# Performance work log

Hardware: AMD Instinct MI355X
Metric: run time of the kernel (lower is better)

Reference implementation:

```python
import jax, jax.numpy as jnp
import numpy as np

IN_DIM, HID, MID, FFN, OUT = 384, 128, 1024, 512, 1024
B, T = 8, 4096
LN_EPS = 1e-5


def _legs_hippo(n: int) -> np.ndarray:
    # A[i, j] = P_i(2j/n - 1) * sqrt(2i + 1), Legendre via 3-term recurrence
    x = 2.0 * np.arange(n) / n - 1.0          # eval points, shape [n]
    P = np.zeros((n, n), dtype=np.float64)     # P[i] = P_i(x)
    P[0] = 1.0
    if n > 1:
        P[1] = x
    for i in range(1, n - 1):
        P[i + 1] = ((2 * i + 1) * x * P[i] - i * P[i - 1]) / (i + 1)
    A = P * np.sqrt(2.0 * np.arange(n) + 1.0)[:, None]
    # rescale so the 4096-step recurrence stays finite (A is a free Parameter,
    # so any test value is valid; unscaled LegS overflows fp32 in ~20 steps)
    s = np.linalg.norm(A, 2)
    return (A / (1.05 * s)).astype(np.float32)


def _layernorm(x, g, b):
    mu = jnp.mean(x, axis=-1, keepdims=True)
    var = jnp.var(x, axis=-1, keepdims=True)
    return (x - mu) * jax.lax.rsqrt(var + LN_EPS) * g + b


def setup_inputs() -> dict:
    key = jax.random.key(0)
    ks = jax.random.split(key, 16)

    def w(k, shape, fan_in):
        return jax.random.normal(k, shape, jnp.float32) * (1.0 / np.sqrt(fan_in))

    return {
        "padded_x": jax.random.normal(ks[0], (B, T, IN_DIM), jnp.float32),
        "seq_lens": jax.random.randint(ks[1], (B,), 1, T + 1, jnp.int32),
        "A": jnp.asarray(_legs_hippo(HID)),
        "enc_w1": w(ks[2], (IN_DIM, MID), IN_DIM), "enc_b1": jnp.zeros((MID,), jnp.float32),
        "enc_w2": w(ks[3], (MID, HID), MID), "enc_b2": jnp.zeros((HID,), jnp.float32),
        "proj_w": w(ks[4], (HID, MID), HID), "proj_b": jnp.zeros((MID,), jnp.float32),
        "ln1_g": jnp.ones((MID,), jnp.float32), "ln1_b": jnp.zeros((MID,), jnp.float32),
        "ffn_w1": w(ks[5], (MID, FFN), MID), "ffn_b1": jnp.zeros((FFN,), jnp.float32),
        "ffn_w2": w(ks[6], (FFN, OUT), FFN), "ffn_b2": jnp.zeros((OUT,), jnp.float32),
        "ln2_g": jnp.ones((OUT,), jnp.float32), "ln2_b": jnp.zeros((OUT,), jnp.float32),
        "out_w": w(ks[7], (OUT, OUT), OUT), "out_b": jnp.zeros((OUT,), jnp.float32),
    }


def reference(padded_x, seq_lens, A, enc_w1, enc_b1, enc_w2, enc_b2,
              proj_w, proj_b, ln1_g, ln1_b, ffn_w1, ffn_b1, ffn_w2, ffn_b2,
              ln2_g, ln2_b, out_w, out_b):
    # encoder: Linear -> GELU(exact) -> Linear   [B, T, HID]
    h_mid = jax.nn.gelu(padded_x @ enc_w1 + enc_b1, approximate=False)
    seqs_bx = h_mid @ enc_w2 + enc_b2

    # masked linear recurrence h_t = A @ h_{t-1} + Bx_t via lax.scan over time
    xs = jnp.swapaxes(seqs_bx, 0, 1)           # [T, B, HID]
    ts = jnp.arange(xs.shape[0])

    def step(h, inp):
        x_t, t = inp
        upd = h @ A.T + x_t                     # (A @ h)^T batched
        mask = (t < seq_lens)[:, None]          # [B, 1]
        return jnp.where(mask, upd, h), None

    h0 = jnp.zeros((padded_x.shape[0], A.shape[0]), padded_x.dtype)
    batch_h, _ = jax.lax.scan(step, h0, (xs, ts))

    # decoder
    projected = batch_h @ proj_w + proj_b
    norm_h = _layernorm(projected, ln1_g, ln1_b)
    ffn_out = jax.nn.gelu(norm_h @ ffn_w1 + ffn_b1, approximate=False) @ ffn_w2 + ffn_b2
    ffn_out = ffn_out + projected               # residual (requires OUT == MID)
    norm_ffn = _layernorm(ffn_out, ln2_g, ln2_b)
    return norm_ffn @ out_w + out_b             # [B, OUT]
```

## Files before the change

kernel.cpp:

```cpp
#include <hip/hip_runtime.h>

typedef __attribute__((ext_vector_type(8))) short short8;
typedef __attribute__((ext_vector_type(4))) short short4v;
typedef __attribute__((ext_vector_type(4))) float float4v;

__device__ __forceinline__ float bf2f(short s) {
  union { float f; unsigned u; } cv; cv.u = ((unsigned)(unsigned short)s) << 16; return cv.f;
}
__device__ __forceinline__ short f2bf(float f) {
  union { float f; unsigned u; } cv; cv.f = f;
  unsigned u = cv.u;
  unsigned r = u + 0x7FFFu + ((u >> 16) & 1u);
  return (short)(r >> 16);
}
__device__ __forceinline__ float gelu_f(float v) {
  return 0.5f * v * (1.0f + erff(v * 0.70710678118654752440f));
}
__device__ __forceinline__ void glds16(const short* g, short* l) {
  __builtin_amdgcn_global_load_lds(
      (const __attribute__((address_space(1))) void*)g,
      (__attribute__((address_space(3))) void*)l, 16, 0, 0);
}

__global__ __launch_bounds__(256) void enc_fused(
    const short* __restrict__ xB, const short* __restrict__ w1T,
    const short* __restrict__ w2T, const float* __restrict__ b1,
    float* __restrict__ encP, const int* __restrict__ seq_lens)
{
  int m0 = blockIdx.x * 64;
  { int b = m0 >> 12, t = m0 & 4095; if (t >= seq_lens[b]) return; }
  int nc0 = blockIdx.y * 2;

  __shared__ __align__(16) short As[64 * 64];
  __shared__ __align__(16) short Ws[128 * 64];
  __shared__ __align__(16) short midb[64 * 128];

  int tid = threadIdx.x, lane = tid & 63, wave = tid >> 6;
  int l15 = lane & 15, quad = lane >> 4;
  int lr = lane >> 3, lseg = lane & 7;

  float4v accO[4][2];
#pragma unroll
  for (int i = 0; i < 4; i++)
#pragma unroll
    for (int j = 0; j < 2; j++) accO[i][j] = 0;

  for (int nci = 0; nci < 2; ++nci) {
    int nc = nc0 + nci;
    float4v accM[4][2];
#pragma unroll
    for (int i = 0; i < 4; i++)
#pragma unroll
      for (int j = 0; j < 2; j++) accM[i][j] = 0;

    for (int ks = 0; ks < 6; ++ks) {
      int kk = ks * 64;
#pragma unroll
      for (int i = 0; i < 2; i++) {
        int rowg = wave * 16 + i * 8;
        glds16(xB + (size_t)(m0 + rowg + lr) * 384 + kk + (lseg ^ lr) * 8, &As[rowg * 64]);
      }
#pragma unroll
      for (int i = 0; i < 4; i++) {
        int rowg = wave * 32 + i * 8;
        glds16(w1T + (size_t)(nc * 128 + rowg + lr) * 384 + kk + (lseg ^ lr) * 8, &Ws[rowg * 64]);
      }
      __syncthreads();
#pragma unroll
      for (int kh = 0; kh < 2; kh++) {
        int s = kh * 4 + quad;
        short8 af[4], bfr[2];
#pragma unroll
        for (int im = 0; im < 4; im++) {
          int r = im * 16 + l15;
          af[im] = *(short8*)&As[r * 64 + ((s ^ (r & 7)) * 8)];
        }
#pragma unroll
        for (int in = 0; in < 2; in++) {
          int r = wave * 32 + in * 16 + l15;
          bfr[in] = *(short8*)&Ws[r * 64 + ((s ^ (r & 7)) * 8)];
        }
#pragma unroll
        for (int im = 0; im < 4; im++)
#pragma unroll
          for (int in = 0; in < 2; in++)
            accM[im][in] = __builtin_amdgcn_mfma_f32_16x16x32_bf16(af[im], bfr[in], accM[im][in], 0, 0, 0);
      }
      __syncthreads();
    }
#pragma unroll
    for (int im = 0; im < 4; im++)
#pragma unroll
      for (int in = 0; in < 2; in++) {
        int k = wave * 32 + in * 16 + l15;
        float bias = b1[nc * 128 + k];
#pragma unroll
        for (int reg = 0; reg < 4; reg++) {
          int m = im * 16 + quad * 4 + reg;
          float v = gelu_f(accM[im][in][reg] + bias);
          int s = k >> 3;
          int sw = (s & 8) | ((s & 7) ^ (m & 7));
          midb[m * 128 + sw * 8 + (k & 7)] = f2bf(v);
        }
      }
    __syncthreads();
#pragma unroll
    for (int ks2 = 0; ks2 < 2; ++ks2) {
      int kk = nc * 128 + ks2 * 64;
#pragma unroll
      for (int i = 0; i < 4; i++) {
        int rowg = wave * 32 + i * 8;
        glds16(w2T + (size_t)(rowg + lr) * 1024 + kk + (lseg ^ lr) * 8, &Ws[rowg * 64]);
      }
      __syncthreads();
#pragma unroll
      for (int kh = 0; kh < 2; kh++) {
        short8 af[4], bfr[2];
#pragma unroll
        for (int im = 0; im < 4; im++) {
          int m = im * 16 + l15;
          int kb = ks2 * 64 + kh * 32 + quad * 8;
          int s = kb >> 3;
          int sw = (s & 8) | ((s & 7) ^ (m & 7));
          af[im] = *(short8*)&midb[m * 128 + sw * 8];
        }
#pragma unroll
        for (int in = 0; in < 2; in++) {
          int r = wave * 32 + in * 16 + l15;
          int s = kh * 4 + quad;
          bfr[in] = *(short8*)&Ws[r * 64 + ((s ^ (r & 7)) * 8)];
        }
#pragma unroll
        for (int im = 0; im < 4; im++)
#pragma unroll
          for (int in = 0; in < 2; in++)
            accO[im][in] = __builtin_amdgcn_mfma_f32_16x16x32_bf16(af[im], bfr[in], accO[im][in], 0, 0, 0);
      }
      __syncthreads();
    }
  }
  float* outp = encP + ((size_t)blockIdx.y << 22);
#pragma unroll
  for (int im = 0; im < 4; im++)
#pragma unroll
    for (int in = 0; in < 2; in++) {
      int n = wave * 32 + in * 16 + l15;
#pragma unroll
      for (int reg = 0; reg < 4; reg++) {
        int m = m0 + im * 16 + quad * 4 + reg;
        outp[(size_t)m * 128 + n] = accO[im][in][reg];
      }
    }
}

__global__ __launch_bounds__(256) void enc_reduce(
    const float* __restrict__ encP, const float* __restrict__ b2,
    short* __restrict__ seqs, const int* __restrict__ seq_lens)
{
  int m0 = blockIdx.x * 64;
  { int b = m0 >> 12, t = m0 & 4095; if (t >= seq_lens[b]) return; }
  int t = threadIdx.x;
#pragma unroll
  for (int i = 0; i < 8; i++) {
    int f4 = t + i * 256;
    int m = m0 + (f4 >> 5);
    int cg = f4 & 31;
    size_t off = (size_t)m * 128 + cg * 4;
    float4v v = *(const float4v*)&encP[off];
#pragma unroll
    for (int y = 1; y < 4; y++) {
      float4v w = *(const float4v*)&encP[((size_t)y << 22) + off];
#pragma unroll
      for (int q = 0; q < 4; q++) v[q] += w[q];
    }
    float4v bb = *(const float4v*)&b2[cg * 4];
    short4v o;
#pragma unroll
    for (int q = 0; q < 4; q++) o[q] = f2bf(v[q] + bb[q]);
    *(short4v*)&seqs[off] = o;
  }
}

__global__ __launch_bounds__(256) void gemm_bt(
    const short* __restrict__ A_, const short* __restrict__ BT,
    float* __restrict__ out, int lda, int ldb, int ldc,
    int kSteps, int kChunk)
{
  int m0 = blockIdx.y * 128;
  int n0 = blockIdx.x * 128;
  int kBase = blockIdx.z * kChunk;

  __shared__ __align__(16) short As[128 * 64];
  __shared__ __align__(16) short Bs[128 * 64];

  int tid = threadIdx.x;
  int lane = tid & 63, wave = tid >> 6;
  int l15 = lane & 15, quad = lane >> 4;
  int wm = wave & 1, wn = wave >> 1;
  int lr = lane >> 3, lseg = lane & 7;

  float4v acc[4][4];
#pragma unroll
  for (int i = 0; i < 4; i++)
#pragma unroll
    for (int j = 0; j < 4; j++) acc[i][j] = 0;

  for (int ks = 0; ks < kSteps; ++ks) {
    int kk = kBase + ks * 64;
#pragma unroll
    for (int i = 0; i < 4; i++) {
      int rowg = wave * 32 + i * 8;
      glds16(A_ + (size_t)(m0 + rowg + lr) * lda + kk + (lseg ^ lr) * 8, &As[rowg * 64]);
      glds16(BT + (size_t)(n0 + rowg + lr) * ldb + kk + (lseg ^ lr) * 8, &Bs[rowg * 64]);
    }
    __syncthreads();
#pragma unroll
    for (int kh = 0; kh < 2; kh++) {
      int s = kh * 4 + quad;
      short8 af[4], bfr[4];
#pragma unroll
      for (int im = 0; im < 4; im++) {
        int r = wm * 64 + im * 16 + l15;
        af[im] = *(short8*)&As[r * 64 + ((s ^ (r & 7)) * 8)];
      }
#pragma unroll
      for (int in = 0; in < 4; in++) {
        int r = wn * 64 + in * 16 + l15;
        bfr[in] = *(short8*)&Bs[r * 64 + ((s ^ (r & 7)) * 8)];
      }
#pragma unroll
      for (int im = 0; im < 4; im++)
#pragma unroll
        for (int in = 0; in < 4; in++)
          acc[im][in] = __builtin_amdgcn_mfma_f32_16x16x32_bf16(af[im], bfr[in], acc[im][in], 0, 0, 0);
    }
    __syncthreads();
  }
  float* outz = out + (size_t)blockIdx.z * 65536;
#pragma unroll
  for (int im = 0; im < 4; im++)
#pragma unroll
    for (int in = 0; in < 4; in++) {
      int n = n0 + wn * 64 + in * 16 + l15;
#pragma unroll
      for (int reg = 0; reg < 4; reg++) {
        int m = m0 + wm * 64 + im * 16 + quad * 4 + reg;
        outz[(size_t)m * ldc + n] = acc[im][in][reg];
      }
    }
}

__global__ void prep_wide(const float* __restrict__ x, const float* __restrict__ w1,
                          const float* __restrict__ w2,
                          const float* __restrict__ proj_w, const float* __restrict__ ffn_w1,
                          const float* __restrict__ ffn_w2, const float* __restrict__ out_w,
                          const float* __restrict__ A, const int* __restrict__ seq_lens,
                          short* __restrict__ xB,
                          short* __restrict__ w1T, short* __restrict__ w2T,
                          short* __restrict__ projB, short* __restrict__ ffn1B,
                          short* __restrict__ ffn2B, short* __restrict__ outB,
                          short* __restrict__ P1, short* __restrict__ P1t,
                          short* __restrict__ P2t,
                          short* __restrict__ Spow, short* __restrict__ SpowT)
{
  int idx = blockIdx.x * 256 + threadIdx.x;
  if (idx < 3145728) {
    int row = idx / 96;
    int t = row & 4095, b = row >> 12;
    if (t >= seq_lens[b]) return;
    float4v v = ((const float4v*)x)[idx];
    short4v o;
#pragma unroll
    for (int j = 0; j < 4; j++) o[j] = f2bf(v[j]);
    ((short4v*)xB)[idx] = o;
    return;
  }
  idx -= 3145728;
  if (idx < 393216) {
    int n = idx / 384, k = idx % 384;
    w1T[idx] = f2bf(w1[k * 1024 + n]);
    return;
  }
  idx -= 393216;
  if (idx < 131072) {
    int n = idx / 1024, k = idx % 1024;
    w2T[idx] = f2bf(w2[k * 128 + n]);
    return;
  }
  idx -= 131072;
  if (idx < 131072) { projB[idx] = f2bf(proj_w[idx]); return; }
  idx -= 131072;
  if (idx < 524288) { ffn1B[idx] = f2bf(ffn_w1[idx]); return; }
  idx -= 524288;
  if (idx < 524288) { ffn2B[idx] = f2bf(ffn_w2[idx]); return; }
  idx -= 524288;
  if (idx < 1048576) { outB[idx] = f2bf(out_w[idx]); return; }
  idx -= 1048576;
  if (idx < 16384) {
    int i = idx >> 7, j = idx & 127;
    short bidv = f2bf((i == j) ? 1.0f : 0.0f);
    P1[i * 8192 + 63 * 128 + j] = bidv;
    P1t[(63 * 128 + j) * 128 + i] = bidv;
    P2t[(63 * 128 + j) * 128 + i] = bidv;
    short ab = f2bf(A[idx]);
    Spow[idx] = ab;
    SpowT[(size_t)j * 128 + i] = ab;
  }
}

__global__ __launch_bounds__(256) void pow_chain(short* __restrict__ Spow,
                                                 short* __restrict__ SpowT)
{
  __shared__ short X[16384];
  __shared__ short XT[16384];
  int t = threadIdx.x;
  for (int i = t * 8; i < 16384; i += 2048) {
    *(short8*)&X[i]  = *(const short8*)&Spow[i];
    *(short8*)&XT[i] = *(const short8*)&SpowT[i];
  }
  __syncthreads();
  int lane = t & 63, wave = t >> 6, l15 = lane & 15, quad = lane >> 4;
  for (int step = 1; step <= 11; ++step) {
    short8 af[2][4], bfr[8][4];
#pragma unroll
    for (int mt = 0; mt < 2; mt++)
#pragma unroll
      for (int ks = 0; ks < 4; ks++)
        af[mt][ks] = *(short8*)&X[(wave * 32 + mt * 16 + l15) * 128 + ks * 32 + quad * 8];
#pragma unroll
    for (int nt = 0; nt < 8; nt++)
#pragma unroll
      for (int ks = 0; ks < 4; ks++)
        bfr[nt][ks] = *(short8*)&XT[(nt * 16 + l15) * 128 + ks * 32 + quad * 8];
    __syncthreads();
    float4v acc[2][8];
#pragma unroll
    for (int mt = 0; mt < 2; mt++)
#pragma unroll
      for (int nt = 0; nt < 8; nt++) acc[mt][nt] = 0;
#pragma unroll
    for (int ks = 0; ks < 4; ks++)
#pragma unroll
      for (int mt = 0; mt < 2; mt++)
#pragma unroll
        for (int nt = 0; nt < 8; nt++)
          acc[mt][nt] = __builtin_amdgcn_mfma_f32_16x16x32_bf16(af[mt][ks], bfr[nt][ks], acc[mt][nt], 0, 0, 0);
    short* gX  = Spow  + (size_t)step * 16384;
    short* gXT = SpowT + (size_t)step * 16384;
#pragma unroll
    for (int mt = 0; mt < 2; mt++)
#pragma unroll
      for (int nt = 0; nt < 8; nt++)
#pragma unroll
        for (int reg = 0; reg < 4; reg++) {
          int m = wave * 32 + mt * 16 + quad * 4 + reg;
          int n = nt * 16 + l15;
          short v = f2bf(acc[mt][nt][reg]);
          X[m * 128 + n] = v; XT[n * 128 + m] = v;
          gX[m * 128 + n] = v; gXT[n * 128 + m] = v;
        }
    __syncthreads();
  }
}

__global__ __launch_bounds__(256) void pow_fill(const short* __restrict__ Spow,
                                                const short* __restrict__ SpowT,
                                                short* __restrict__ P1,
                                                short* __restrict__ P1t,
                                                short* __restrict__ P2t)
{
  __shared__ short cur[16384];
  __shared__ short Bt[16384];
  int bid = blockIdx.x;
  int table1 = bid < 63;
  int e = table1 ? bid + 1 : bid - 62;
  int t = threadIdx.x;
  int lane = t & 63, wave = t >> 6, l15 = lane & 15, quad = lane >> 4;

  int bits = e;
  int k0 = __ffs(bits) - 1; bits &= bits - 1;
  int s0 = table1 ? k0 : (k0 == 0 ? 6 : 6 + k0);
  for (int i = t * 8; i < 16384; i += 2048)
    *(short8*)&cur[i] = *(const short8*)&Spow[(size_t)s0 * 16384 + i];

  while (bits) {
    int k = __ffs(bits) - 1; bits &= bits - 1;
    int si = table1 ? k : (k == 0 ? 6 : 6 + k);
    for (int i = t * 8; i < 16384; i += 2048)
      *(short8*)&Bt[i] = *(const short8*)&SpowT[(size_t)si * 16384 + i];
    __syncthreads();
    short8 af[2][4], bfr[8][4];
#pragma unroll
    for (int mt = 0; mt < 2; mt++)
#pragma unroll
      for (int ks = 0; ks < 4; ks++)
        af[mt][ks] = *(short8*)&cur[(wave * 32 + mt * 16 + l15) * 128 + ks * 32 + quad * 8];
#pragma unroll
    for (int nt = 0; nt < 8; nt++)
#pragma unroll
      for (int ks = 0; ks < 4; ks++)
        bfr[nt][ks] = *(short8*)&Bt[(nt * 16 + l15) * 128 + ks * 32 + quad * 8];
    __syncthreads();
    float4v acc[2][8];
#pragma unroll
    for (int mt = 0; mt < 2; mt++)
#pragma unroll
      for (int nt = 0; nt < 8; nt++) acc[mt][nt] = 0;
#pragma unroll
    for (int ks = 0; ks < 4; ks++)
#pragma unroll
      for (int mt = 0; mt < 2; mt++)
#pragma unroll
        for (int nt = 0; nt < 8; nt++)
          acc[mt][nt] = __builtin_amdgcn_mfma_f32_16x16x32_bf16(af[mt][ks], bfr[nt][ks], acc[mt][nt], 0, 0, 0);
#pragma unroll
    for (int mt = 0; mt < 2; mt++)
#pragma unroll
      for (int nt = 0; nt < 8; nt++)
#pragma unroll
        for (int reg = 0; reg < 4; reg++) {
          int m = wave * 32 + mt * 16 + quad * 4 + reg;
          int n = nt * 16 + l15;
          cur[m * 128 + n] = f2bf(acc[mt][nt][reg]);
        }
    __syncthreads();
  }
  __syncthreads();
  int slot = 63 - e;
  for (int idx = t; idx < 16384; idx += 256) {
    int i = idx >> 7, j = idx & 127;
    short v = cur[idx];
    if (table1) {
      P1[i * 8192 + slot * 128 + j] = v;
      P1t[(slot * 128 + j) * 128 + i] = v;
    } else {
      P2t[(slot * 128 + j) * 128 + i] = v;
    }
  }
}

__global__ __launch_bounds__(256) void combine_gemm(
    const float* __restrict__ Vz, const short* __restrict__ seqs,
    const int* __restrict__ seq_lens,
    const short* __restrict__ P2t, const short* __restrict__ P1t,
    float* __restrict__ hFtail)
{
  __shared__ short X[256 * 8];
  int pp = blockIdx.x >> 5, ks = blockIdx.x & 31;
  int t = threadIdx.x;
  for (int e = t; e < 2048; e += 256) {
    int klocal = e >> 3, b = e & 7;
    int cp = ks * 2 + (klocal >> 7), i = klocal & 127;
    int L = seq_lens[b];
    if (pp == 0) {
      int F = L >> 6, sh = 64 - F;
      float v = 0.f;
      if (cp >= sh) {
        int row = (b * 64 + (cp - sh)) * 128 + i;
#pragma unroll
        for (int z = 0; z < 32; z++) v += Vz[(size_t)z * 65536 + row];
      }
      X[e] = f2bf(v);
    } else {
      int F = L >> 6, rr = L & 63, sh = 64 - rr;
      short s = 0;
      if (cp >= sh) s = seqs[((size_t)b * 4096 + F * 64 + (cp - sh)) * 128 + i];
      X[e] = s;
    }
  }
  __syncthreads();
  const short* P = pp ? P1t : P2t;
  float* outp = hFtail + pp * 1024;
  int i = t & 127, g = t >> 7;
  float acc[4] = {0, 0, 0, 0};
  for (int kl = 0; kl < 256; ++kl) {
    int k = ks * 256 + kl;
    float pv = bf2f(P[k * 128 + i]);
    short4v xv = *(const short4v*)(X + kl * 8 + g * 4);
#pragma unroll
    for (int q = 0; q < 4; q++) acc[q] += bf2f(xv[q]) * pv;
  }
#pragma unroll
  for (int q = 0; q < 4; q++) atomicAdd(&outp[(g * 4 + q) * 128 + i], acc[q]);
}

__global__ __launch_bounds__(256) void proj_stage(
    const float* __restrict__ hFtail, const short* __restrict__ P1t,
    const int* __restrict__ seq_lens, const short* __restrict__ projB,
    const float* __restrict__ proj_b, float* __restrict__ projected)
{
  __shared__ short hT[128 * 8];
  __shared__ float red[4][64][8];
  int t = threadIdx.x;
  {
    int b = t >> 5, i4 = (t & 31) * 4;
    int rr = seq_lens[b] & 63;
    const short* M = P1t + (size_t)(63 - rr) * 128 * 128;
    const float* hF = hFtail + b * 128;
    float acc[4];
#pragma unroll
    for (int q = 0; q < 4; q++) acc[q] = hFtail[1024 + b * 128 + i4 + q];
    for (int j = 0; j < 128; ++j) {
      float hv = hF[j];
      short4v mv = *(const short4v*)&M[j * 128 + i4];
#pragma unroll
      for (int q = 0; q < 4; q++) acc[q] += bf2f(mv[q]) * hv;
    }
#pragma unroll
    for (int q = 0; q < 4; q++) hT[(i4 + q) * 8 + b] = f2bf(acc[q]);
  }
  __syncthreads();
  int c = t & 63, sl = t >> 6;
  int n = blockIdx.x * 64 + c;
  float acc[8] = {0, 0, 0, 0, 0, 0, 0, 0};
  for (int k = sl * 32; k < sl * 32 + 32; ++k) {
    short8 xv = *(short8*)&hT[k * 8];
    float wv = bf2f(projB[k * 1024 + n]);
#pragma unroll
    for (int b = 0; b < 8; b++) acc[b] += bf2f(xv[b]) * wv;
  }
#pragma unroll
  for (int b = 0; b < 8; b++) red[sl][c][b] = acc[b];
  __syncthreads();
  if (sl == 0) {
#pragma unroll
    for (int s = 1; s < 4; s++)
#pragma unroll
      for (int b = 0; b < 8; b++) acc[b] += red[s][c][b];
    float bn = proj_b[n];
#pragma unroll
    for (int b = 0; b < 8; b++) projected[b * 1024 + n] = acc[b] + bn;
  }
}

__global__ __launch_bounds__(256) void ffn1_stage(
    const float* __restrict__ projected, const float* __restrict__ g1,
    const float* __restrict__ b1, const short* __restrict__ ffn1B,
    float* __restrict__ ffn1raw)
{
  __shared__ float part[8][32][2];
  __shared__ float stats[8][2];
  __shared__ short xT[256 * 8];
  __shared__ float red[4][64][8];
  int t = threadIdx.x;
  { int b = t >> 5, j0 = t & 31; float s = 0, q = 0;
    for (int k = j0 * 32; k < j0 * 32 + 32; ++k) { float v = projected[b * 1024 + k]; s += v; q += v * v; }
    part[b][j0][0] = s; part[b][j0][1] = q; }
  __syncthreads();
  if (t < 8) {
    float s = 0, q = 0;
    for (int j = 0; j < 32; j++) { s += part[t][j][0]; q += part[t][j][1]; }
    float mu = s * (1.0f / 1024.0f);
    float var = q * (1.0f / 1024.0f) - mu * mu;
    stats[t][0] = mu; stats[t][1] = rsqrtf(var + 1e-5f);
  }
  __syncthreads();
  int ky0 = blockIdx.y * 256;
  for (int idx = t; idx < 2048; idx += 256) {
    int kl = idx >> 3, b = idx & 7; int k = ky0 + kl;
    float v = (projected[b * 1024 + k] - stats[b][0]) * stats[b][1] * g1[k] + b1[k];
    xT[kl * 8 + b] = f2bf(v);
  }
  __syncthreads();
  int c = t & 63, sl = t >> 6;
  int n = blockIdx.x * 64 + c;
  float acc[8] = {0, 0, 0, 0, 0, 0, 0, 0};
  for (int kl = sl * 64; kl < sl * 64 + 64; ++kl) {
    short8 xv = *(short8*)&xT[kl * 8];
    float wv = bf2f(ffn1B[(size_t)(ky0 + kl) * 512 + n]);
#pragma unroll
    for (int b = 0; b < 8; b++) acc[b] += bf2f(xv[b]) * wv;
  }
#pragma unroll
  for (int b = 0; b < 8; b++) red[sl][c][b] = acc[b];
  __syncthreads();
  if (sl == 0) {
#pragma unroll
    for (int s = 1; s < 4; s++)
#pragma unroll
      for (int b = 0; b < 8; b++) acc[b] += red[s][c][b];
#pragma unroll
    for (int b = 0; b < 8; b++) atomicAdd(&ffn1raw[b * 512 + n], acc[b]);
  }
}

__global__ __launch_bounds__(256) void ffn2_stage(
    const float* __restrict__ ffn1raw, const float* __restrict__ fb1,
    const short* __restrict__ ffn2B, float* __restrict__ ffn2raw)
{
  __shared__ short xT[256 * 8];
  __shared__ float red[4][64][8];
  int t = threadIdx.x;
  int ky0 = blockIdx.y * 256;
  for (int idx = t; idx < 2048; idx += 256) {
    int kl = idx >> 3, b = idx & 7; int k = ky0 + kl;
    float v = gelu_f(ffn1raw[b * 512 + k] + fb1[k]);
    xT[kl * 8 + b] = f2bf(v);
  }
  __syncthreads();
  int c = t & 63, sl = t >> 6;
  int n = blockIdx.x * 64 + c;
  float acc[8] = {0, 0, 0, 0, 0, 0, 0, 0};
  for (int kl = sl * 64; kl < sl * 64 + 64; ++kl) {
    short8 xv = *(short8*)&xT[kl * 8];
    float wv = bf2f(ffn2B[(size_t)(ky0 + kl) * 1024 + n]);
#pragma unroll
    for (int b = 0; b < 8; b++) acc[b] += bf2f(xv[b]) * wv;
  }
#pragma unroll
  for (int b = 0; b < 8; b++) red[sl][c][b] = acc[b];
  __syncthreads();
  if (sl == 0) {
#pragma unroll
    for (int s = 1; s < 4; s++)
#pragma unroll
      for (int b = 0; b < 8; b++) acc[b] += red[s][c][b];
#pragma unroll
    for (int b = 0; b < 8; b++) atomicAdd(&ffn2raw[b * 1024 + n], acc[b]);
  }
}

__global__ __launch_bounds__(256) void out_stage(
    const float* __restrict__ ffn2raw, const float* __restrict__ fb2,
    const float* __restrict__ projected, const float* __restrict__ g2,
    const float* __restrict__ b2ln, const short* __restrict__ outB,
    const float* __restrict__ out_b, float* __restrict__ d_out)
{
  __shared__ float part[8][32][2];
  __shared__ float stats[8][2];
  __shared__ short xT[512 * 8];
  __shared__ float red[4][64][8];
  int t = threadIdx.x;
  { int b = t >> 5, j0 = t & 31; float s = 0, q = 0;
    for (int k = j0 * 32; k < j0 * 32 + 32; ++k) {
      float v = ffn2raw[b * 1024 + k] + fb2[k] + projected[b * 1024 + k];
      s += v; q += v * v;
    }
    part[b][j0][0] = s; part[b][j0][1] = q; }
  __syncthreads();
  if (t < 8) {
    float s = 0, q = 0;
    for (int j = 0; j < 32; j++) { s += part[t][j][0]; q += part[t][j][1]; }
    float mu = s * (1.0f / 1024.0f);
    float var = q * (1.0f / 1024.0f) - mu * mu;
    stats[t][0] = mu; stats[t][1] = rsqrtf(var + 1e-5f);
  }
  __syncthreads();
  int ky0 = blockIdx.y * 512;
  for (int idx = t; idx < 4096; idx += 256) {
    int kl = idx >> 3, b = idx & 7; int k = ky0 + kl;
    float v = ffn2raw[b * 1024 + k] + fb2[k] + projected[b * 1024 + k];
    v = (v - stats[b][0]) * stats[b][1] * g2[k] + b2ln[k];
    xT[kl * 8 + b] = f2bf(v);
  }
  __syncthreads();
  int c = t & 63, sl = t >> 6;
  int n = blockIdx.x * 64 + c;
  float acc[8] = {0, 0, 0, 0, 0, 0, 0, 0};
  for (int kl = sl * 128; kl < sl * 128 + 128; ++kl) {
    short8 xv = *(short8*)&xT[kl * 8];
    float wv = bf2f(outB[(size_t)(ky0 + kl) * 1024 + n]);
#pragma unroll
    for (int b = 0; b < 8; b++) acc[b] += bf2f(xv[b]) * wv;
  }
#pragma unroll
  for (int b = 0; b < 8; b++) red[sl][c][b] = acc[b];
  __syncthreads();
  if (sl == 0) {
#pragma unroll
    for (int s = 1; s < 4; s++)
#pragma unroll
      for (int b = 0; b < 8; b++) acc[b] += red[s][c][b];
    float bn = (blockIdx.y == 0) ? out_b[n] : 0.0f;
#pragma unroll
    for (int b = 0; b < 8; b++) atomicAdd(&d_out[b * 1024 + n], acc[b] + bn);
  }
}

extern "C" void kernel_launch(void* const* d_in, const int* in_sizes, int n_in,
                              void* d_out, int out_size, void* d_ws, size_t ws_size,
                              hipStream_t stream)
{
  (void)in_sizes; (void)n_in; (void)out_size; (void)ws_size;
  const float* x      = (const float*)d_in[0];
  const int* seq_lens = (const int*)d_in[1];
  const float* A      = (const float*)d_in[2];
  const float* enc_w1 = (const float*)d_in[3];
  const float* enc_b1 = (const float*)d_in[4];
  const float* enc_w2 = (const float*)d_in[5];
  const float* enc_b2 = (const float*)d_in[6];
  const float* proj_w = (const float*)d_in[7];
  const float* proj_b = (const float*)d_in[8];
  const float* ln1_g  = (const float*)d_in[9];
  const float* ln1_b  = (const float*)d_in[10];
  const float* ffn_w1 = (const float*)d_in[11];
  const float* ffn_b1 = (const float*)d_in[12];
  const float* ffn_w2 = (const float*)d_in[13];
  const float* ffn_b2 = (const float*)d_in[14];
  const float* ln2_g  = (const float*)d_in[15];
  const float* ln2_b  = (const float*)d_in[16];
  const float* out_w  = (const float*)d_in[17];
  const float* out_b  = (const float*)d_in[18];

  char* p = (char*)d_ws;
  auto alloc = [&](size_t bytes) { char* r = p; p += (bytes + 255) & ~(size_t)255; return r; };
  short* xB    = (short*)alloc(32768ull * 384 * 2);
  float* encP  = (float*)alloc(4ull * 32768 * 128 * 4);
  short* seqs  = (short*)alloc(32768ull * 128 * 2);
  short* w1T   = (short*)alloc(1024ull * 384 * 2);
  short* w2T   = (short*)alloc(128ull * 1024 * 2);
  short* projB = (short*)alloc(128ull * 1024 * 2);
  short* ffn1B = (short*)alloc(1024ull * 512 * 2);
  short* ffn2B = (short*)alloc(512ull * 1024 * 2);
  short* outB  = (short*)alloc(1024ull * 1024 * 2);
  short* Spow  = (short*)alloc(12ull * 16384 * 2);
  short* SpowT = (short*)alloc(12ull * 16384 * 2);
  short* P1    = (short*)alloc(128ull * 8192 * 2);
  short* P1t   = (short*)alloc(8192ull * 128 * 2);
  short* P2t   = (short*)alloc(8192ull * 128 * 2);
  float* Vz    = (float*)alloc(32ull * 512 * 128 * 4);
  float* hFtail  = (float*)alloc(2ull * 8 * 128 * 4);
  float* ffn1raw = (float*)alloc(8ull * 512 * 4);
  float* ffn2raw = (float*)alloc(8ull * 1024 * 4);
  float* projected = (float*)alloc(8ull * 1024 * 4);

  hipMemsetAsync(hFtail, 0, (2ull * 8 * 128 + 8ull * 512 + 8ull * 1024) * 4, stream);
  hipMemsetAsync(d_out, 0, 8192ull * 4, stream);

  prep_wide<<<23104, 256, 0, stream>>>(x, enc_w1, enc_w2, proj_w, ffn_w1, ffn_w2, out_w, A,
      seq_lens, xB, w1T, w2T, projB, ffn1B, ffn2B, outB, P1, P1t, P2t, Spow, SpowT);
  pow_chain<<<1, 256, 0, stream>>>(Spow, SpowT);
  pow_fill<<<126, 256, 0, stream>>>(Spow, SpowT, P1, P1t, P2t);

  enc_fused<<<dim3(512, 4), 256, 0, stream>>>(xB, w1T, w2T, enc_b1, encP, seq_lens);
  enc_reduce<<<512, 256, 0, stream>>>(encP, enc_b2, seqs, seq_lens);

  gemm_bt<<<dim3(1, 4, 32), 256, 0, stream>>>(seqs, P1, Vz, 8192, 8192, 128, 4, 256);
  combine_gemm<<<64, 256, 0, stream>>>(Vz, seqs, seq_lens, P2t, P1t, hFtail);

  proj_stage<<<16, 256, 0, stream>>>(hFtail, P1t, seq_lens, projB, proj_b, projected);
  ffn1_stage<<<dim3(8, 4), 256, 0, stream>>>(projected, ln1_g, ln1_b, ffn1B, ffn1raw);
  ffn2_stage<<<dim3(16, 2), 256, 0, stream>>>(ffn1raw, ffn_b1, ffn2B, ffn2raw);
  out_stage<<<dim3(16, 2), 256, 0, stream>>>(ffn2raw, ffn_b2, projected, ln2_g, ln2_b,
      outB, out_b, (float*)d_out);
}
```

Before: 405.4 us.

## Fuse encoder reduce into last block, drop memsets, widen decoder grids

Several changes land together. The encoder split-N reduction is folded into enc_fused: the last of the four column blocks per row tile, found with an atomic counter, sums the partials and writes the bf16 sequence, which removes the enc_reduce launch. The two memsets are replaced by zeroing inside prep_wide, and the encoder's shared memory is reduced by aliasing the input tile onto the mid buffer. The decoder GEMV stages and combine_gemm are split across more blocks with smaller K chunks to raise parallelism, and the pow_chain/pow_fill transposed stores are vectorized or coalesced. The cost is extra atomics, threadfences and more atomicAdd traffic into the outputs.

```diff
diff --git a/kernel.cpp b/kernel.cpp
--- a/kernel.cpp
+++ b/kernel.cpp
@@ -20,234 +20,6 @@
   __builtin_amdgcn_global_load_lds(
       (const __attribute__((address_space(1))) void*)g,
       (__attribute__((address_space(3))) void*)l, 16, 0, 0);
-}
-
-__global__ __launch_bounds__(256) void enc_fused(
-    const short* __restrict__ xB, const short* __restrict__ w1T,
-    const short* __restrict__ w2T, const float* __restrict__ b1,
-    float* __restrict__ encP, const int* __restrict__ seq_lens)
-{
-  int m0 = blockIdx.x * 64;
-  { int b = m0 >> 12, t = m0 & 4095; if (t >= seq_lens[b]) return; }
-  int nc0 = blockIdx.y * 2;
-
-  __shared__ __align__(16) short As[64 * 64];
-  __shared__ __align__(16) short Ws[128 * 64];
-  __shared__ __align__(16) short midb[64 * 128];
-
-  int tid = threadIdx.x, lane = tid & 63, wave = tid >> 6;
-  int l15 = lane & 15, quad = lane >> 4;
-  int lr = lane >> 3, lseg = lane & 7;
-
-  float4v accO[4][2];
-#pragma unroll
-  for (int i = 0; i < 4; i++)
-#pragma unroll
-    for (int j = 0; j < 2; j++) accO[i][j] = 0;
-
-  for (int nci = 0; nci < 2; ++nci) {
-    int nc = nc0 + nci;
-    float4v accM[4][2];
-#pragma unroll
-    for (int i = 0; i < 4; i++)
-#pragma unroll
-      for (int j = 0; j < 2; j++) accM[i][j] = 0;
-
-    for (int ks = 0; ks < 6; ++ks) {
-      int kk = ks * 64;
-#pragma unroll
-      for (int i = 0; i < 2; i++) {
-        int rowg = wave * 16 + i * 8;
-        glds16(xB + (size_t)(m0 + rowg + lr) * 384 + kk + (lseg ^ lr) * 8, &As[rowg * 64]);
-      }
-#pragma unroll
-      for (int i = 0; i < 4; i++) {
-        int rowg = wave * 32 + i * 8;
-        glds16(w1T + (size_t)(nc * 128 + rowg + lr) * 384 + kk + (lseg ^ lr) * 8, &Ws[rowg * 64]);
-      }
-      __syncthreads();
-#pragma unroll
-      for (int kh = 0; kh < 2; kh++) {
-        int s = kh * 4 + quad;
-        short8 af[4], bfr[2];
-#pragma unroll
-        for (int im = 0; im < 4; im++) {
-          int r = im * 16 + l15;
-          af[im] = *(short8*)&As[r * 64 + ((s ^ (r & 7)) * 8)];
-        }
-#pragma unroll
-        for (int in = 0; in < 2; in++) {
-          int r = wave * 32 + in * 16 + l15;
-          bfr[in] = *(short8*)&Ws[r * 64 + ((s ^ (r & 7)) * 8)];
-        }
-#pragma unroll
-        for (int im = 0; im < 4; im++)
-#pragma unroll
-          for (int in = 0; in < 2; in++)
-            accM[im][in] = __builtin_amdgcn_mfma_f32_16x16x32_bf16(af[im], bfr[in], accM[im][in], 0, 0, 0);
-      }
-      __syncthreads();
-    }
-#pragma unroll
-    for (int im = 0; im < 4; im++)
-#pragma unroll
-      for (int in = 0; in < 2; in++) {
-        int k = wave * 32 + in * 16 + l15;
-        float bias = b1[nc * 128 + k];
-#pragma unroll
-        for (int reg = 0; reg < 4; reg++) {
-          int m = im * 16 + quad * 4 + reg;
-          float v = gelu_f(accM[im][in][reg] + bias);
-          int s = k >> 3;
-          int sw = (s & 8) | ((s & 7) ^ (m & 7));
-          midb[m * 128 + sw * 8 + (k & 7)] = f2bf(v);
-        }
-      }
-    __syncthreads();
-#pragma unroll
-    for (int ks2 = 0; ks2 < 2; ++ks2) {
-      int kk = nc * 128 + ks2 * 64;
-#pragma unroll
-      for (int i = 0; i < 4; i++) {
-        int rowg = wave * 32 + i * 8;
-        glds16(w2T + (size_t)(rowg + lr) * 1024 + kk + (lseg ^ lr) * 8, &Ws[rowg * 64]);
-      }
-      __syncthreads();
-#pragma unroll
-      for (int kh = 0; kh < 2; kh++) {
-        short8 af[4], bfr[2];
-#pragma unroll
-        for (int im = 0; im < 4; im++) {
-          int m = im * 16 + l15;
-          int kb = ks2 * 64 + kh * 32 + quad * 8;
-          int s = kb >> 3;
-          int sw = (s & 8) | ((s & 7) ^ (m & 7));
-          af[im] = *(short8*)&midb[m * 128 + sw * 8];
-        }
-#pragma unroll
-        for (int in = 0; in < 2; in++) {
-          int r = wave * 32 + in * 16 + l15;
-          int s = kh * 4 + quad;
-          bfr[in] = *(short8*)&Ws[r * 64 + ((s ^ (r & 7)) * 8)];
-        }
-#pragma unroll
-        for (int im = 0; im < 4; im++)
-#pragma unroll
-          for (int in = 0; in < 2; in++)
-            accO[im][in] = __builtin_amdgcn_mfma_f32_16x16x32_bf16(af[im], bfr[in], accO[im][in], 0, 0, 0);
-      }
-      __syncthreads();
-    }
-  }
-  float* outp = encP + ((size_t)blockIdx.y << 22);
-#pragma unroll
-  for (int im = 0; im < 4; im++)
-#pragma unroll
-    for (int in = 0; in < 2; in++) {
-      int n = wave * 32 + in * 16 + l15;
-#pragma unroll
-      for (int reg = 0; reg < 4; reg++) {
-        int m = m0 + im * 16 + quad * 4 + reg;
-        outp[(size_t)m * 128 + n] = accO[im][in][reg];
-      }
-    }
-}
-
-__global__ __launch_bounds__(256) void enc_reduce(
-    const float* __restrict__ encP, const float* __restrict__ b2,
-    short* __restrict__ seqs, const int* __restrict__ seq_lens)
-{
-  int m0 = blockIdx.x * 64;
-  { int b = m0 >> 12, t = m0 & 4095; if (t >= seq_lens[b]) return; }
-  int t = threadIdx.x;
-#pragma unroll
-  for (int i = 0; i < 8; i++) {
-    int f4 = t + i * 256;
-    int m = m0 + (f4 >> 5);
-    int cg = f4 & 31;
-    size_t off = (size_t)m * 128 + cg * 4;
-    float4v v = *(const float4v*)&encP[off];
-#pragma unroll
-    for (int y = 1; y < 4; y++) {
-      float4v w = *(const float4v*)&encP[((size_t)y << 22) + off];
-#pragma unroll
-      for (int q = 0; q < 4; q++) v[q] += w[q];
-    }
-    float4v bb = *(const float4v*)&b2[cg * 4];
-    short4v o;
-#pragma unroll
-    for (int q = 0; q < 4; q++) o[q] = f2bf(v[q] + bb[q]);
-    *(short4v*)&seqs[off] = o;
-  }
-}
-
-__global__ __launch_bounds__(256) void gemm_bt(
-    const short* __restrict__ A_, const short* __restrict__ BT,
-    float* __restrict__ out, int lda, int ldb, int ldc,
-    int kSteps, int kChunk)
-{
-  int m0 = blockIdx.y * 128;
-  int n0 = blockIdx.x * 128;
-  int kBase = blockIdx.z * kChunk;
-
-  __shared__ __align__(16) short As[128 * 64];
-  __shared__ __align__(16) short Bs[128 * 64];
-
-  int tid = threadIdx.x;
-  int lane = tid & 63, wave = tid >> 6;
-  int l15 = lane & 15, quad = lane >> 4;
-  int wm = wave & 1, wn = wave >> 1;
-  int lr = lane >> 3, lseg = lane & 7;
-
-  float4v acc[4][4];
-#pragma unroll
-  for (int i = 0; i < 4; i++)
-#pragma unroll
-    for (int j = 0; j < 4; j++) acc[i][j] = 0;
-
-  for (int ks = 0; ks < kSteps; ++ks) {
-    int kk = kBase + ks * 64;
-#pragma unroll
-    for (int i = 0; i < 4; i++) {
-      int rowg = wave * 32 + i * 8;
-      glds16(A_ + (size_t)(m0 + rowg + lr) * lda + kk + (lseg ^ lr) * 8, &As[rowg * 64]);
-      glds16(BT + (size_t)(n0 + rowg + lr) * ldb + kk + (lseg ^ lr) * 8, &Bs[rowg * 64]);
-    }
-    __syncthreads();
-#pragma unroll
-    for (int kh = 0; kh < 2; kh++) {
-      int s = kh * 4 + quad;
-      short8 af[4], bfr[4];
-#pragma unroll
-      for (int im = 0; im < 4; im++) {
-        int r = wm * 64 + im * 16 + l15;
-        af[im] = *(short8*)&As[r * 64 + ((s ^ (r & 7)) * 8)];
-      }
-#pragma unroll
-      for (int in = 0; in < 4; in++) {
-        int r = wn * 64 + in * 16 + l15;
-        bfr[in] = *(short8*)&Bs[r * 64 + ((s ^ (r & 7)) * 8)];
-      }
-#pragma unroll
-      for (int im = 0; im < 4; im++)
-#pragma unroll
-        for (int in = 0; in < 4; in++)
-          acc[im][in] = __builtin_amdgcn_mfma_f32_16x16x32_bf16(af[im], bfr[in], acc[im][in], 0, 0, 0);
-    }
-    __syncthreads();
-  }
-  float* outz = out + (size_t)blockIdx.z * 65536;
-#pragma unroll
-  for (int im = 0; im < 4; im++)
-#pragma unroll
-    for (int in = 0; in < 4; in++) {
-      int n = n0 + wn * 64 + in * 16 + l15;
-#pragma unroll
-      for (int reg = 0; reg < 4; reg++) {
-        int m = m0 + wm * 64 + im * 16 + quad * 4 + reg;
-        outz[(size_t)m * ldc + n] = acc[im][in][reg];
-      }
-    }
 }
 
 __global__ void prep_wide(const float* __restrict__ x, const float* __restrict__ w1,
@@ -261,7 +33,10 @@
                           short* __restrict__ ffn2B, short* __restrict__ outB,
                           short* __restrict__ P1, short* __restrict__ P1t,
                           short* __restrict__ P2t,
-                          short* __restrict__ Spow, short* __restrict__ SpowT)
+                          short* __restrict__ Spow, short* __restrict__ SpowT,
+                          float* __restrict__ hFtail, float* __restrict__ ffn1raw,
+                          float* __restrict__ ffn2raw, float* __restrict__ dout0,
+                          int* __restrict__ encCnt)
 {
   int idx = blockIdx.x * 256 + threadIdx.x;
   if (idx < 3145728) {
@@ -298,13 +73,183 @@
   idx -= 1048576;
   if (idx < 16384) {
     int i = idx >> 7, j = idx & 127;
-    short bidv = f2bf((i == j) ? 1.0f : 0.0f);
-    P1[i * 8192 + 63 * 128 + j] = bidv;
-    P1t[(63 * 128 + j) * 128 + i] = bidv;
-    P2t[(63 * 128 + j) * 128 + i] = bidv;
+    short idv = f2bf((i == j) ? 1.0f : 0.0f);
+    P1[i * 8192 + 63 * 128 + j] = idv;
+    P1t[(63 * 128 + j) * 128 + i] = idv;
+    P2t[(63 * 128 + j) * 128 + i] = idv;
     short ab = f2bf(A[idx]);
     Spow[idx] = ab;
     SpowT[(size_t)j * 128 + i] = ab;
+    return;
+  }
+  idx -= 16384;
+  if (idx < 2048) { hFtail[idx] = 0.f; return; }
+  idx -= 2048;
+  if (idx < 4096) { ffn1raw[idx] = 0.f; return; }
+  idx -= 4096;
+  if (idx < 8192) { ffn2raw[idx] = 0.f; return; }
+  idx -= 8192;
+  if (idx < 8192) { dout0[idx] = 0.f; return; }
+  idx -= 8192;
+  if (idx < 512) encCnt[idx] = 0;
+}
+
+__global__ __launch_bounds__(256) void enc_fused(
+    const short* __restrict__ xB, const short* __restrict__ w1T,
+    const short* __restrict__ w2T, const float* __restrict__ b1,
+    const float* __restrict__ b2, float* __restrict__ encP,
+    short* __restrict__ seqs, int* __restrict__ encCnt,
+    const int* __restrict__ seq_lens)
+{
+  int m0 = blockIdx.x * 64;
+  { int b = m0 >> 12, t = m0 & 4095; if (t >= seq_lens[b]) return; }
+  int nc0 = blockIdx.y * 2;
+
+  __shared__ __align__(16) short Ws[128 * 64];
+  __shared__ __align__(16) short Mb[64 * 128];
+  short* As = Mb;
+  __shared__ int lastf;
+
+  int tid = threadIdx.x, lane = tid & 63, wave = tid >> 6;
+  int l15 = lane & 15, quad = lane >> 4;
+  int lr = lane >> 3, lseg = lane & 7;
+
+  float4v accO[4][2];
+#pragma unroll
+  for (int i = 0; i < 4; i++)
+#pragma unroll
+    for (int j = 0; j < 2; j++) accO[i][j] = 0;
+
+  for (int nci = 0; nci < 2; ++nci) {
+    int nc = nc0 + nci;
+    float4v accM[4][2];
+#pragma unroll
+    for (int i = 0; i < 4; i++)
+#pragma unroll
+      for (int j = 0; j < 2; j++) accM[i][j] = 0;
+
+    for (int ks = 0; ks < 6; ++ks) {
+      int kk = ks * 64;
+#pragma unroll
+      for (int i = 0; i < 2; i++) {
+        int rowg = wave * 16 + i * 8;
+        glds16(xB + (size_t)(m0 + rowg + lr) * 384 + kk + (lseg ^ lr) * 8, &As[rowg * 64]);
+      }
+#pragma unroll
+      for (int i = 0; i < 4; i++) {
+        int rowg = wave * 32 + i * 8;
+        glds16(w1T + (size_t)(nc * 128 + rowg + lr) * 384 + kk + (lseg ^ lr) * 8, &Ws[rowg * 64]);
+      }
+      __syncthreads();
+#pragma unroll
+      for (int kh = 0; kh < 2; kh++) {
+        int s = kh * 4 + quad;
+        short8 af[4], bfr[2];
+#pragma unroll
+        for (int im = 0; im < 4; im++) {
+          int r = im * 16 + l15;
+          af[im] = *(short8*)&As[r * 64 + ((s ^ (r & 7)) * 8)];
+        }
+#pragma unroll
+        for (int in = 0; in < 2; in++) {
+          int r = wave * 32 + in * 16 + l15;
+          bfr[in] = *(short8*)&Ws[r * 64 + ((s ^ (r & 7)) * 8)];
+        }
+#pragma unroll
+        for (int im = 0; im < 4; im++)
+#pragma unroll
+          for (int in = 0; in < 2; in++)
+            accM[im][in] = __builtin_amdgcn_mfma_f32_16x16x32_bf16(af[im], bfr[in], accM[im][in], 0, 0, 0);
+      }
+      __syncthreads();
+    }
+#pragma unroll
+    for (int im = 0; im < 4; im++)
+#pragma unroll
+      for (int in = 0; in < 2; in++) {
+        int k = wave * 32 + in * 16 + l15;
+        float bias = b1[nc * 128 + k];
+#pragma unroll
+        for (int reg = 0; reg < 4; reg++) {
+          int m = im * 16 + quad * 4 + reg;
+          float v = gelu_f(accM[im][in][reg] + bias);
+          int s = k >> 3;
+          int sw = (s & 8) | ((s & 7) ^ (m & 7));
+          Mb[m * 128 + sw * 8 + (k & 7)] = f2bf(v);
+        }
+      }
+    __syncthreads();
+#pragma unroll
+    for (int ks2 = 0; ks2 < 2; ++ks2) {
+      int kk = nc * 128 + ks2 * 64;
+#pragma unroll
+      for (int i = 0; i < 4; i++) {
+        int rowg = wave * 32 + i * 8;
+        glds16(w2T + (size_t)(rowg + lr) * 1024 + kk + (lseg ^ lr) * 8, &Ws[rowg * 64]);
+      }
+      __syncthreads();
+#pragma unroll
+      for (int kh = 0; kh < 2; kh++) {
+        short8 af[4], bfr[2];
+#pragma unroll
+        for (int im = 0; im < 4; im++) {
+          int m = im * 16 + l15;
+          int kb = ks2 * 64 + kh * 32 + quad * 8;
+          int s = kb >> 3;
+          int sw = (s & 8) | ((s & 7) ^ (m & 7));
+          af[im] = *(short8*)&Mb[m * 128 + sw * 8];
+        }
+#pragma unroll
+        for (int in = 0; in < 2; in++) {
+          int r = wave * 32 + in * 16 + l15;
+          int s = kh * 4 + quad;
+          bfr[in] = *(short8*)&Ws[r * 64 + ((s ^ (r & 7)) * 8)];
+        }
+#pragma unroll
+        for (int im = 0; im < 4; im++)
+#pragma unroll
+          for (int in = 0; in < 2; in++)
+            accO[im][in] = __builtin_amdgcn_mfma_f32_16x16x32_bf16(af[im], bfr[in], accO[im][in], 0, 0, 0);
+      }
+      __syncthreads();
+    }
+  }
+  float* outp = encP + ((size_t)blockIdx.y << 22);
+#pragma unroll
+  for (int im = 0; im < 4; im++)
+#pragma unroll
+    for (int in = 0; in < 2; in++) {
+      int n = wave * 32 + in * 16 + l15;
+#pragma unroll
+      for (int reg = 0; reg < 4; reg++) {
+        int m = m0 + im * 16 + quad * 4 + reg;
+        outp[(size_t)m * 128 + n] = accO[im][in][reg];
+      }
+    }
+  __threadfence();
+  if (tid == 0) lastf = (atomicAdd(&encCnt[blockIdx.x], 1) == 3);
+  __syncthreads();
+  if (lastf) {
+    __threadfence();
+#pragma unroll
+    for (int i = 0; i < 8; i++) {
+      int f4 = tid + i * 256;
+      int m = m0 + (f4 >> 5);
+      int cg = f4 & 31;
+      size_t off = (size_t)m * 128 + cg * 4;
+      float4v v = *(const float4v*)&encP[off];
+#pragma unroll
+      for (int y = 1; y < 4; y++) {
+        float4v w = *(const float4v*)&encP[((size_t)y << 22) + off];
+#pragma unroll
+        for (int q = 0; q < 4; q++) v[q] += w[q];
+      }
+      float4v bb = *(const float4v*)&b2[cg * 4];
+      short4v o;
+#pragma unroll
+      for (int q = 0; q < 4; q++) o[q] = f2bf(v[q] + bb[q]);
+      *(short4v*)&seqs[off] = o;
+    }
   }
 }
 
@@ -350,15 +295,20 @@
 #pragma unroll
     for (int mt = 0; mt < 2; mt++)
 #pragma unroll
-      for (int nt = 0; nt < 8; nt++)
+      for (int nt = 0; nt < 8; nt++) {
+        int n = nt * 16 + l15;
+        int mbase = wave * 32 + mt * 16 + quad * 4;
+        short4v pk;
 #pragma unroll
         for (int reg = 0; reg < 4; reg++) {
-          int m = wave * 32 + mt * 16 + quad * 4 + reg;
-          int n = nt * 16 + l15;
           short v = f2bf(acc[mt][nt][reg]);
-          X[m * 128 + n] = v; XT[n * 128 + m] = v;
-          gX[m * 128 + n] = v; gXT[n * 128 + m] = v;
+          pk[reg] = v;
+          X[(mbase + reg) * 128 + n] = v;
+          gX[(mbase + reg) * 128 + n] = v;
         }
+        *(short4v*)&XT[n * 128 + mbase] = pk;
+        *(short4v*)&gXT[n * 128 + mbase] = pk;
+      }
     __syncthreads();
   }
 }
@@ -427,16 +377,90 @@
   }
   __syncthreads();
   int slot = 63 - e;
-  for (int idx = t; idx < 16384; idx += 256) {
-    int i = idx >> 7, j = idx & 127;
-    short v = cur[idx];
-    if (table1) {
-      P1[i * 8192 + slot * 128 + j] = v;
-      P1t[(slot * 128 + j) * 128 + i] = v;
-    } else {
-      P2t[(slot * 128 + j) * 128 + i] = v;
-    }
-  }
+  if (table1) {
+    for (int idx = t; idx < 16384; idx += 256) {
+      int i = idx >> 7, j = idx & 127;
+      P1[i * 8192 + slot * 128 + j] = cur[idx];
+    }
+    for (int idx = t; idx < 16384; idx += 256) {
+      int j = idx >> 7, r = idx & 127;
+      P1t[(slot * 128 + j) * 128 + r] = cur[r * 128 + j];
+    }
+  } else {
+    for (int idx = t; idx < 16384; idx += 256) {
+      int j = idx >> 7, r = idx & 127;
+      P2t[(slot * 128 + j) * 128 + r] = cur[r * 128 + j];
+    }
+  }
+}
+
+__global__ __launch_bounds__(256) void gemm_bt(
+    const short* __restrict__ A_, const short* __restrict__ BT,
+    float* __restrict__ out, int lda, int ldb, int ldc,
+    int kSteps, int kChunk)
+{
+  int m0 = blockIdx.y * 128;
+  int n0 = blockIdx.x * 128;
+  int kBase = blockIdx.z * kChunk;
+
+  __shared__ __align__(16) short As[128 * 64];
+  __shared__ __align__(16) short Bs[128 * 64];
+
+  int tid = threadIdx.x;
+  int lane = tid & 63, wave = tid >> 6;
+  int l15 = lane & 15, quad = lane >> 4;
+  int wm = wave & 1, wn = wave >> 1;
+  int lr = lane >> 3, lseg = lane & 7;
+
+  float4v acc[4][4];
+#pragma unroll
+  for (int i = 0; i < 4; i++)
+#pragma unroll
+    for (int j = 0; j < 4; j++) acc[i][j] = 0;
+
+  for (int ks = 0; ks < kSteps; ++ks) {
+    int kk = kBase + ks * 64;
+#pragma unroll
+    for (int i = 0; i < 4; i++) {
+      int rowg = wave * 32 + i * 8;
+      glds16(A_ + (size_t)(m0 + rowg + lr) * lda + kk + (lseg ^ lr) * 8, &As[rowg * 64]);
+      glds16(BT + (size_t)(n0 + rowg + lr) * ldb + kk + (lseg ^ lr) * 8, &Bs[rowg * 64]);
+    }
+    __syncthreads();
+#pragma unroll
+    for (int kh = 0; kh < 2; kh++) {
+      int s = kh * 4 + quad;
+      short8 af[4], bfr[4];
+#pragma unroll
+      for (int im = 0; im < 4; im++) {
+        int r = wm * 64 + im * 16 + l15;
+        af[im] = *(short8*)&As[r * 64 + ((s ^ (r & 7)) * 8)];
+      }
+#pragma unroll
+      for (int in = 0; in < 4; in++) {
+        int r = wn * 64 + in * 16 + l15;
+        bfr[in] = *(short8*)&Bs[r * 64 + ((s ^ (r & 7)) * 8)];
+      }
+#pragma unroll
+      for (int im = 0; im < 4; im++)
+#pragma unroll
+        for (int in = 0; in < 4; in++)
+          acc[im][in] = __builtin_amdgcn_mfma_f32_16x16x32_bf16(af[im], bfr[in], acc[im][in], 0, 0, 0);
+    }
+    __syncthreads();
+  }
+  float* outz = out + (size_t)blockIdx.z * 65536;
+#pragma unroll
+  for (int im = 0; im < 4; im++)
+#pragma unroll
+    for (int in = 0; in < 4; in++) {
+      int n = n0 + wn * 64 + in * 16 + l15;
+#pragma unroll
+      for (int reg = 0; reg < 4; reg++) {
+        int m = m0 + wm * 64 + im * 16 + quad * 4 + reg;
+        outz[(size_t)m * ldc + n] = acc[im][in][reg];
+      }
+    }
 }
 
 __global__ __launch_bounds__(256) void combine_gemm(
@@ -445,12 +469,11 @@
     const short* __restrict__ P2t, const short* __restrict__ P1t,
     float* __restrict__ hFtail)
 {
-  __shared__ short X[256 * 8];
-  int pp = blockIdx.x >> 5, ks = blockIdx.x & 31;
+  __shared__ short X[128 * 8];
+  int pp = blockIdx.x >> 6, cp = blockIdx.x & 63;
   int t = threadIdx.x;
-  for (int e = t; e < 2048; e += 256) {
-    int klocal = e >> 3, b = e & 7;
-    int cp = ks * 2 + (klocal >> 7), i = klocal & 127;
+  for (int e = t; e < 1024; e += 256) {
+    int i = e >> 3, b = e & 7;
     int L = seq_lens[b];
     if (pp == 0) {
       int F = L >> 6, sh = 64 - F;
@@ -473,8 +496,8 @@
   float* outp = hFtail + pp * 1024;
   int i = t & 127, g = t >> 7;
   float acc[4] = {0, 0, 0, 0};
-  for (int kl = 0; kl < 256; ++kl) {
-    int k = ks * 256 + kl;
+  for (int kl = 0; kl < 128; ++kl) {
+    int k = cp * 128 + kl;
     float pv = bf2f(P[k * 128 + i]);
     short4v xv = *(const short4v*)(X + kl * 8 + g * 4);
 #pragma unroll
@@ -495,7 +518,7 @@
   {
     int b = t >> 5, i4 = (t & 31) * 4;
     int rr = seq_lens[b] & 63;
-    const short* M = P1t + (size_t)(63 - rr) * 128 * 128;
+    const short* M = P1t + (size_t)(63 - rr) * 16384;
     const float* hF = hFtail + b * 128;
     float acc[4];
 #pragma unroll
@@ -540,7 +563,7 @@
 {
   __shared__ float part[8][32][2];
   __shared__ float stats[8][2];
-  __shared__ short xT[256 * 8];
+  __shared__ short xT[64 * 8];
   __shared__ float red[4][64][8];
   int t = threadIdx.x;
   { int b = t >> 5, j0 = t & 31; float s = 0, q = 0;
@@ -555,8 +578,8 @@
     stats[t][0] = mu; stats[t][1] = rsqrtf(var + 1e-5f);
   }
   __syncthreads();
-  int ky0 = blockIdx.y * 256;
-  for (int idx = t; idx < 2048; idx += 256) {
+  int ky0 = blockIdx.y * 64;
+  for (int idx = t; idx < 512; idx += 256) {
     int kl = idx >> 3, b = idx & 7; int k = ky0 + kl;
     float v = (projected[b * 1024 + k] - stats[b][0]) * stats[b][1] * g1[k] + b1[k];
     xT[kl * 8 + b] = f2bf(v);
@@ -565,7 +588,7 @@
   int c = t & 63, sl = t >> 6;
   int n = blockIdx.x * 64 + c;
   float acc[8] = {0, 0, 0, 0, 0, 0, 0, 0};
-  for (int kl = sl * 64; kl < sl * 64 + 64; ++kl) {
+  for (int kl = sl * 16; kl < sl * 16 + 16; ++kl) {
     short8 xv = *(short8*)&xT[kl * 8];
     float wv = bf2f(ffn1B[(size_t)(ky0 + kl) * 512 + n]);
 #pragma unroll
@@ -588,11 +611,11 @@
     const float* __restrict__ ffn1raw, const float* __restrict__ fb1,
     const short* __restrict__ ffn2B, float* __restrict__ ffn2raw)
 {
-  __shared__ short xT[256 * 8];
+  __shared__ short xT[64 * 8];
   __shared__ float red[4][64][8];
   int t = threadIdx.x;
-  int ky0 = blockIdx.y * 256;
-  for (int idx = t; idx < 2048; idx += 256) {
+  int ky0 = blockIdx.y * 64;
+  for (int idx = t; idx < 512; idx += 256) {
     int kl = idx >> 3, b = idx & 7; int k = ky0 + kl;
     float v = gelu_f(ffn1raw[b * 512 + k] + fb1[k]);
     xT[kl * 8 + b] = f2bf(v);
@@ -601,7 +624,7 @@
   int c = t & 63, sl = t >> 6;
   int n = blockIdx.x * 64 + c;
   float acc[8] = {0, 0, 0, 0, 0, 0, 0, 0};
-  for (int kl = sl * 64; kl < sl * 64 + 64; ++kl) {
+  for (int kl = sl * 16; kl < sl * 16 + 16; ++kl) {
     short8 xv = *(short8*)&xT[kl * 8];
     float wv = bf2f(ffn2B[(size_t)(ky0 + kl) * 1024 + n]);
 #pragma unroll
@@ -628,7 +651,7 @@
 {
   __shared__ float part[8][32][2];
   __shared__ float stats[8][2];
-  __shared__ short xT[512 * 8];
+  __shared__ short xT[128 * 8];
   __shared__ float red[4][64][8];
   int t = threadIdx.x;
   { int b = t >> 5, j0 = t & 31; float s = 0, q = 0;
@@ -646,8 +669,8 @@
     stats[t][0] = mu; stats[t][1] = rsqrtf(var + 1e-5f);
   }
   __syncthreads();
-  int ky0 = blockIdx.y * 512;
-  for (int idx = t; idx < 4096; idx += 256) {
+  int ky0 = blockIdx.y * 128;
+  for (int idx = t; idx < 1024; idx += 256) {
     int kl = idx >> 3, b = idx & 7; int k = ky0 + kl;
     float v = ffn2raw[b * 1024 + k] + fb2[k] + projected[b * 1024 + k];
     v = (v - stats[b][0]) * stats[b][1] * g2[k] + b2ln[k];
@@ -657,7 +680,7 @@
   int c = t & 63, sl = t >> 6;
   int n = blockIdx.x * 64 + c;
   float acc[8] = {0, 0, 0, 0, 0, 0, 0, 0};
-  for (int kl = sl * 128; kl < sl * 128 + 128; ++kl) {
+  for (int kl = sl * 32; kl < sl * 32 + 32; ++kl) {
     short8 xv = *(short8*)&xT[kl * 8];
     float wv = bf2f(outB[(size_t)(ky0 + kl) * 1024 + n]);
 #pragma unroll
@@ -719,28 +742,28 @@
   short* P1t   = (short*)alloc(8192ull * 128 * 2);
   short* P2t   = (short*)alloc(8192ull * 128 * 2);
   float* Vz    = (float*)alloc(32ull * 512 * 128 * 4);
-  float* hFtail  = (float*)alloc(2ull * 8 * 128 * 4);
+  float* hFtail  = (float*)alloc(2048ull * 4);
   float* ffn1raw = (float*)alloc(8ull * 512 * 4);
   float* ffn2raw = (float*)alloc(8ull * 1024 * 4);
   float* projected = (float*)alloc(8ull * 1024 * 4);
-
-  hipMemsetAsync(hFtail, 0, (2ull * 8 * 128 + 8ull * 512 + 8ull * 1024) * 4, stream);
-  hipMemsetAsync(d_out, 0, 8192ull * 4, stream);
-
-  prep_wide<<<23104, 256, 0, stream>>>(x, enc_w1, enc_w2, proj_w, ffn_w1, ffn_w2, out_w, A,
-      seq_lens, xB, w1T, w2T, projB, ffn1B, ffn2B, outB, P1, P1t, P2t, Spow, SpowT);
+  int*   encCnt  = (int*)alloc(512ull * 4);
+
+  prep_wide<<<23194, 256, 0, stream>>>(x, enc_w1, enc_w2, proj_w, ffn_w1, ffn_w2, out_w,
+      A, seq_lens, xB, w1T, w2T, projB, ffn1B, ffn2B, outB, P1, P1t, P2t,
+      Spow, SpowT, hFtail, ffn1raw, ffn2raw, (float*)d_out, encCnt);
+
   pow_chain<<<1, 256, 0, stream>>>(Spow, SpowT);
   pow_fill<<<126, 256, 0, stream>>>(Spow, SpowT, P1, P1t, P2t);
 
-  enc_fused<<<dim3(512, 4), 256, 0, stream>>>(xB, w1T, w2T, enc_b1, encP, seq_lens);
-  enc_reduce<<<512, 256, 0, stream>>>(encP, enc_b2, seqs, seq_lens);
+  enc_fused<<<dim3(512, 4), 256, 0, stream>>>(xB, w1T, w2T, enc_b1, enc_b2,
+      encP, seqs, encCnt, seq_lens);
 
   gemm_bt<<<dim3(1, 4, 32), 256, 0, stream>>>(seqs, P1, Vz, 8192, 8192, 128, 4, 256);
-  combine_gemm<<<64, 256, 0, stream>>>(Vz, seqs, seq_lens, P2t, P1t, hFtail);
+  combine_gemm<<<128, 256, 0, stream>>>(Vz, seqs, seq_lens, P2t, P1t, hFtail);
 
   proj_stage<<<16, 256, 0, stream>>>(hFtail, P1t, seq_lens, projB, proj_b, projected);
-  ffn1_stage<<<dim3(8, 4), 256, 0, stream>>>(projected, ln1_g, ln1_b, ffn1B, ffn1raw);
-  ffn2_stage<<<dim3(16, 2), 256, 0, stream>>>(ffn1raw, ffn_b1, ffn2B, ffn2raw);
-  out_stage<<<dim3(16, 2), 256, 0, stream>>>(ffn2raw, ffn_b2, projected, ln2_g, ln2_b,
+  ffn1_stage<<<dim3(8, 16), 256, 0, stream>>>(projected, ln1_g, ln1_b, ffn1B, ffn1raw);
+  ffn2_stage<<<dim3(16, 8), 256, 0, stream>>>(ffn1raw, ffn_b1, ffn2B, ffn2raw);
+  out_stage<<<dim3(16, 8), 256, 0, stream>>>(ffn2raw, ffn_b2, projected, ln2_g, ln2_b,
       outB, out_b, (float*)d_out);
 }
```

After: 493.4 us. 1.22x slower.
